# Kernel tuning notes

Measured on AMD Instinct MI355X. Metric: run time of the kernel, lower is better.

## Reference

```python
import jax, jax.numpy as jnp
import numpy as np

B, C, H, W, N = 16, 81, 128, 128, 64


def setup_inputs() -> dict:
    key = jax.random.key(0)
    k1, k2, k3, k4, k5 = jax.random.split(key, 5)
    bbox_pred = jax.random.normal(k1, (B, 4, H, W), jnp.float32)
    class_pred = jax.random.normal(k2, (B, C, H, W), jnp.float32)
    # well-formed GT boxes in [0,1]: x1y1 + positive wh
    xy = jax.random.uniform(k3, (B, N, 2), jnp.float32)
    wh = jax.random.uniform(k4, (B, N, 2), jnp.float32) * 0.5 + 0.05
    boxes = jnp.concatenate([xy, xy + wh], axis=-1)  # [B,N,4]
    labels = jax.random.randint(k5, (B, N), 0, C).astype(jnp.int32)
    return {"bbox_pred": bbox_pred, "class_pred": class_pred,
            "boxes": boxes, "labels": labels}


def reference(bbox_pred, class_pred, boxes, labels):
    Bb, Cc, Hh, Ww = class_pred.shape
    A = Hh * Ww
    pb = bbox_pred.transpose(0, 2, 3, 1).reshape(Bb, A, 4)   # [B,A,4]
    pc = class_pred.transpose(0, 2, 3, 1).reshape(Bb, A, Cc)  # [B,A,C]

    # pairwise IoU [B,A,N] via broadcasting (pred [B,A,1,4] vs gt [B,1,N,4])
    p = pb[:, :, None, :]
    g = boxes[:, None, :, :]
    ix1 = jnp.maximum(p[..., 0], g[..., 0])
    iy1 = jnp.maximum(p[..., 1], g[..., 1])
    ix2 = jnp.minimum(p[..., 2], g[..., 2])
    iy2 = jnp.minimum(p[..., 3], g[..., 3])
    inter = jnp.clip(ix2 - ix1, 0) * jnp.clip(iy2 - iy1, 0)
    pa = (pb[..., 2] - pb[..., 0]) * (pb[..., 3] - pb[..., 1])      # [B,A]
    ga = (boxes[..., 2] - boxes[..., 0]) * (boxes[..., 3] - boxes[..., 1])  # [B,N]
    union = pa[:, :, None] + ga[:, None, :] - inter
    ious = inter / union

    max_ious = ious.max(axis=-1)            # [B,A]
    max_idx = jnp.argmax(ious, axis=-1)     # [B,A]
    pos = max_ious > 0.5                    # [B,A]
    posf = pos.astype(pc.dtype)
    npos = posf.sum(axis=-1)                # [B]
    denom = jnp.maximum(npos, 1.0)

    assigned_labels = jnp.take_along_axis(labels, max_idx, axis=1)          # [B,A]
    assigned_boxes = jnp.take_along_axis(boxes, max_idx[..., None], axis=1)  # [B,A,4]

    # cross-entropy per anchor (mean over positives)
    logp = jax.nn.log_softmax(pc, axis=-1)
    ce = -jnp.take_along_axis(logp, assigned_labels[..., None], axis=2)[..., 0]
    cls_loss = (ce * posf).sum(axis=-1) / denom

    # smooth-L1 (beta=1), mean over positive elements (npos*4)
    diff = pb - assigned_boxes
    ad = jnp.abs(diff)
    sl1 = jnp.where(ad < 1.0, 0.5 * diff * diff, ad - 0.5)
    reg_loss = (sl1 * posf[..., None]).sum(axis=(-1, -2)) / (denom * 4.0)

    # fallback when an image has zero positives: CE with all-zero labels
    zero_loss = -logp[..., 0].mean(axis=-1)

    per_img = jnp.where(npos > 0, cls_loss + reg_loss, zero_loss)
    return per_img.mean()
```

## Files before the change

kernel.cpp:

```cpp
#include <hip/hip_runtime.h>
#include <math.h>

#define Bc 16
#define Cc 81
#define AA 16384
#define Nn 64
#define TPB 256
#define BLOCKS_PER_IMG (AA / TPB)
#define NBLOCKS (Bc * BLOCKS_PER_IMG)
#define G 9
#define NG 9

__global__ __launch_bounds__(TPB) void det_loss_main(
    const float* __restrict__ bbox_pred,
    const float* __restrict__ class_pred,
    const float* __restrict__ boxes,
    const int* __restrict__ labels,
    float4* __restrict__ ws_part)
{
    __shared__ float4 sbox[Nn];
    __shared__ float  sga[Nn];
    __shared__ int    slab[Nn];

    const int blk  = blockIdx.x;
    const int b    = blk / BLOCKS_PER_IMG;
    const int ablk = blk % BLOCKS_PER_IMG;
    const int t    = threadIdx.x;

    if (t < Nn) {
        float4 g = ((const float4*)boxes)[b * Nn + t];
        sbox[t] = g;
        sga[t]  = (g.z - g.x) * (g.w - g.y);
        slab[t] = labels[b * Nn + t];
    }
    __syncthreads();

    const int a = ablk * TPB + t;

    const float* bp = bbox_pred + (size_t)b * 4 * AA + a;
    const float px1 = bp[0 * AA];
    const float py1 = bp[1 * AA];
    const float px2 = bp[2 * AA];
    const float py2 = bp[3 * AA];
    const float pa  = (px2 - px1) * (py2 - py1);

    const float* cp = class_pred + (size_t)b * Cc * AA + a;
    float buf0[G], buf1[G];
#pragma unroll
    for (int k = 0; k < G; ++k) buf0[k] = cp[(size_t)k * AA];

    float best = -INFINITY;
    int   bj   = 0;
#pragma unroll 8
    for (int j = 0; j < Nn; ++j) {
        const float4 g  = sbox[j];
        const float ix1 = fmaxf(px1, g.x);
        const float iy1 = fmaxf(py1, g.y);
        const float ix2 = fminf(px2, g.z);
        const float iy2 = fminf(py2, g.w);
        const float inter = fmaxf(ix2 - ix1, 0.0f) * fmaxf(iy2 - iy1, 0.0f);
        const float iou = inter * __builtin_amdgcn_rcpf(pa + sga[j] - inter);
        if (iou > best) { best = iou; bj = j; }
    }
    const float posf = (best > 0.5f) ? 1.0f : 0.0f;
    const int    lab = slab[bj];
    const float4 gb  = sbox[bj];

    float sA = 0.0f, sB = 0.0f, x0 = 0.0f, xl = 0.0f;
#pragma unroll
    for (int g = 0; g < NG; ++g) {
        if (g + 1 < NG) {
            if ((g & 1) == 0) {
#pragma unroll
                for (int k = 0; k < G; ++k)
                    buf1[k] = cp[(size_t)((g + 1) * G + k) * AA];
            } else {
#pragma unroll
                for (int k = 0; k < G; ++k)
                    buf0[k] = cp[(size_t)((g + 1) * G + k) * AA];
            }
        }
#pragma unroll
        for (int k = 0; k < G; ++k) {
            const float x = ((g & 1) == 0) ? buf0[k] : buf1[k];
            const int   c = g * G + k;
            if (c == 0) x0 = x;
            xl = (c == lab) ? x : xl;
            if (k & 1) sB += __expf(x);
            else       sA += __expf(x);
        }
    }
    const float lse   = __logf(sA + sB);
    const float ce    = (lse - xl) * posf;
    const float logp0 = x0 - lse;

    float sl = 0.0f;
    {
        const float d0 = px1 - gb.x, d1 = py1 - gb.y, d2 = px2 - gb.z, d3 = py2 - gb.w;
        const float a0 = fabsf(d0), a1 = fabsf(d1), a2 = fabsf(d2), a3 = fabsf(d3);
        sl += (a0 < 1.0f) ? 0.5f * d0 * d0 : a0 - 0.5f;
        sl += (a1 < 1.0f) ? 0.5f * d1 * d1 : a1 - 0.5f;
        sl += (a2 < 1.0f) ? 0.5f * d2 * d2 : a2 - 0.5f;
        sl += (a3 < 1.0f) ? 0.5f * d3 * d3 : a3 - 0.5f;
        sl *= posf;
    }

    float v0 = posf, v1 = ce, v2 = sl, v3 = logp0;
#pragma unroll
    for (int o = 32; o > 0; o >>= 1) {
        v0 += __shfl_down(v0, o);
        v1 += __shfl_down(v1, o);
        v2 += __shfl_down(v2, o);
        v3 += __shfl_down(v3, o);
    }
    __shared__ float4 red[4];
    const int wave = t >> 6, lane = t & 63;
    if (lane == 0) red[wave] = make_float4(v0, v1, v2, v3);
    __syncthreads();
    if (t == 0) {
        float4 r0 = red[0], r1 = red[1], r2 = red[2], r3 = red[3];
        ws_part[blk] = make_float4(r0.x + r1.x + r2.x + r3.x,
                                   r0.y + r1.y + r2.y + r3.y,
                                   r0.z + r1.z + r2.z + r3.z,
                                   r0.w + r1.w + r2.w + r3.w);
    }
}

__global__ __launch_bounds__(256) void det_loss_final(
    const float4* __restrict__ ws_part, float* __restrict__ out)
{
    const int t = threadIdx.x;
    float4 p0 = ws_part[t];
    float4 p1 = ws_part[t + 256];
    float4 p2 = ws_part[t + 512];
    float4 p3 = ws_part[t + 768];
#pragma unroll
    for (int o = 1; o < 64; o <<= 1) {
        p0.x += __shfl_xor(p0.x, o); p0.y += __shfl_xor(p0.y, o);
        p0.z += __shfl_xor(p0.z, o); p0.w += __shfl_xor(p0.w, o);
        p1.x += __shfl_xor(p1.x, o); p1.y += __shfl_xor(p1.y, o);
        p1.z += __shfl_xor(p1.z, o); p1.w += __shfl_xor(p1.w, o);
        p2.x += __shfl_xor(p2.x, o); p2.y += __shfl_xor(p2.y, o);
        p2.z += __shfl_xor(p2.z, o); p2.w += __shfl_xor(p2.w, o);
        p3.x += __shfl_xor(p3.x, o); p3.y += __shfl_xor(p3.y, o);
        p3.z += __shfl_xor(p3.z, o); p3.w += __shfl_xor(p3.w, o);
    }
    __shared__ float4 simg[16];
    const int lane = t & 63, w = t >> 6;
    if (lane == 0) {
        simg[w]      = p0;
        simg[w + 4]  = p1;
        simg[w + 8]  = p2;
        simg[w + 12] = p3;
    }
    __syncthreads();
    float per = 0.0f;
    if (t < Bc) {
        const float4 s = simg[t];
        const float npos = s.x;
        const float denom = fmaxf(npos, 1.0f);
        const float cls_reg = s.y / denom + s.z / (denom * 4.0f);
        const float zero_loss = -s.w / (float)AA;
        per = (npos > 0.0f) ? cls_reg : zero_loss;
    }
#pragma unroll
    for (int o = 8; o > 0; o >>= 1) per += __shfl_down(per, o);
    if (t == 0) out[0] = per * (1.0f / (float)Bc);
}

extern "C" void kernel_launch(void* const* d_in, const int* in_sizes, int n_in,
                              void* d_out, int out_size, void* d_ws, size_t ws_size,
                              hipStream_t stream) {
    const float* bbox_pred  = (const float*)d_in[0];
    const float* class_pred = (const float*)d_in[1];
    const float* boxes      = (const float*)d_in[2];
    const int*   labels     = (const int*)d_in[3];
    float* out = (float*)d_out;
    float4* ws = (float4*)d_ws;

    det_loss_main<<<NBLOCKS, TPB, 0, stream>>>(bbox_pred, class_pred, boxes, labels, ws);
    det_loss_final<<<1, 256, 0, stream>>>(ws, out);
}
```

Before: 24.49 us.

## Stream class logits through LDS with async global_load_lds double buffering

Replaces per-thread register-buffered strided loads of the 81 class rows with async global-to-LDS copies (16-byte per lane) into a double-buffered 16-row chunk in shared memory, synchronized via manual waitcnt and barriers. The first two chunks are issued before the IoU loop so the logit loads overlap the IoU computation, and the last row is loaded directly. This frees registers and widens the load granularity, but adds 32KB of LDS per block and block-wide barriers, which may reduce occupancy.

```diff
diff --git a/kernel.cpp b/kernel.cpp
--- a/kernel.cpp
+++ b/kernel.cpp
@@ -8,8 +8,22 @@
 #define TPB 256
 #define BLOCKS_PER_IMG (AA / TPB)
 #define NBLOCKS (Bc * BLOCKS_PER_IMG)
-#define G 9
-#define NG 9
+#define CHROWS 16
+#define NCHUNK 5
+
+__device__ __forceinline__ void issue_chunk(const float* __restrict__ cp_anchor,
+                                            float (*chk)[CHROWS][TPB],
+                                            int ci, int bi, int w, int l) {
+#pragma unroll
+    for (int r = 0; r < 4; ++r) {
+        const int c = ci * CHROWS + 4 * w + r;
+        const float* gp = cp_anchor + (size_t)c * AA + 4 * l;
+        __builtin_amdgcn_global_load_lds(
+            (const __attribute__((address_space(1))) unsigned int*)gp,
+            (__attribute__((address_space(3))) unsigned int*)&chk[bi][4 * w + r][0],
+            16, 0, 0);
+    }
+}
 
 __global__ __launch_bounds__(TPB) void det_loss_main(
     const float* __restrict__ bbox_pred,
@@ -21,11 +35,16 @@
     __shared__ float4 sbox[Nn];
     __shared__ float  sga[Nn];
     __shared__ int    slab[Nn];
+    __shared__ __align__(16) float chk[2][CHROWS][TPB];
+    __shared__ float4 red[4];
 
     const int blk  = blockIdx.x;
     const int b    = blk / BLOCKS_PER_IMG;
     const int ablk = blk % BLOCKS_PER_IMG;
     const int t    = threadIdx.x;
+    const int w    = t >> 6;
+    const int l    = t & 63;
+    const int base = ablk * TPB;
 
     if (t < Nn) {
         float4 g = ((const float4*)boxes)[b * Nn + t];
@@ -35,19 +54,18 @@
     }
     __syncthreads();
 
-    const int a = ablk * TPB + t;
-
-    const float* bp = bbox_pred + (size_t)b * 4 * AA + a;
+    const float* bp = bbox_pred + (size_t)b * 4 * AA + base + t;
     const float px1 = bp[0 * AA];
     const float py1 = bp[1 * AA];
     const float px2 = bp[2 * AA];
     const float py2 = bp[3 * AA];
     const float pa  = (px2 - px1) * (py2 - py1);
 
-    const float* cp = class_pred + (size_t)b * Cc * AA + a;
-    float buf0[G], buf1[G];
-#pragma unroll
-    for (int k = 0; k < G; ++k) buf0[k] = cp[(size_t)k * AA];
+    const float* cp_anchor = class_pred + (size_t)b * Cc * AA + base;
+    issue_chunk(cp_anchor, chk, 0, 0, w, l);
+    issue_chunk(cp_anchor, chk, 1, 1, w, l);
+    __builtin_amdgcn_sched_barrier(0);
+    const float x80 = cp_anchor[(size_t)80 * AA + t];
 
     float best = -INFINITY;
     int   bj   = 0;
@@ -66,30 +84,43 @@
     const int    lab = slab[bj];
     const float4 gb  = sbox[bj];
 
+    asm volatile("s_waitcnt vmcnt(4)" ::: "memory");
+    __builtin_amdgcn_sched_barrier(0);
+    __builtin_amdgcn_s_barrier();
+    __builtin_amdgcn_sched_barrier(0);
+
     float sA = 0.0f, sB = 0.0f, x0 = 0.0f, xl = 0.0f;
 #pragma unroll
-    for (int g = 0; g < NG; ++g) {
-        if (g + 1 < NG) {
-            if ((g & 1) == 0) {
-#pragma unroll
-                for (int k = 0; k < G; ++k)
-                    buf1[k] = cp[(size_t)((g + 1) * G + k) * AA];
-            } else {
-#pragma unroll
-                for (int k = 0; k < G; ++k)
-                    buf0[k] = cp[(size_t)((g + 1) * G + k) * AA];
-            }
-        }
-#pragma unroll
-        for (int k = 0; k < G; ++k) {
-            const float x = ((g & 1) == 0) ? buf0[k] : buf1[k];
-            const int   c = g * G + k;
+    for (int i = 0; i < 4; ++i) {
+#pragma unroll
+        for (int r = 0; r < CHROWS; ++r) {
+            const float x = chk[i & 1][r][t];
+            const int   c = i * CHROWS + r;
             if (c == 0) x0 = x;
             xl = (c == lab) ? x : xl;
-            if (k & 1) sB += __expf(x);
+            if (r & 1) sB += __expf(x);
             else       sA += __expf(x);
         }
-    }
+        __builtin_amdgcn_s_barrier();
+        __builtin_amdgcn_sched_barrier(0);
+        if (i < 3) issue_chunk(cp_anchor, chk, i + 2, i & 1, w, l);
+        if (i < 3) asm volatile("s_waitcnt vmcnt(4)" ::: "memory");
+        else       asm volatile("s_waitcnt vmcnt(0)" ::: "memory");
+        __builtin_amdgcn_sched_barrier(0);
+        __builtin_amdgcn_s_barrier();
+        __builtin_amdgcn_sched_barrier(0);
+    }
+#pragma unroll
+    for (int r = 0; r < CHROWS; ++r) {
+        const float x = chk[0][r][t];
+        const int   c = 4 * CHROWS + r;
+        xl = (c == lab) ? x : xl;
+        if (r & 1) sB += __expf(x);
+        else       sA += __expf(x);
+    }
+    xl = (lab == 80) ? x80 : xl;
+    sA += __expf(x80);
+
     const float lse   = __logf(sA + sB);
     const float ce    = (lse - xl) * posf;
     const float logp0 = x0 - lse;
@@ -113,9 +144,7 @@
         v2 += __shfl_down(v2, o);
         v3 += __shfl_down(v3, o);
     }
-    __shared__ float4 red[4];
-    const int wave = t >> 6, lane = t & 63;
-    if (lane == 0) red[wave] = make_float4(v0, v1, v2, v3);
+    if (l == 0) red[w] = make_float4(v0, v1, v2, v3);
     __syncthreads();
     if (t == 0) {
         float4 r0 = red[0], r1 = red[1], r2 = red[2], r3 = red[3];
```

Result: slower. 26.89 us (+9.8%).

## Split class dimension across two thread halves per anchor to double parallelism

Applied to the files above, without the earlier changes.

Each block now covers 128 anchors with 256 threads. Two waves split the 81 classes (40 and 41 each) for the same anchors and combine partial sum-exp and label logit through shared memory. This doubles the thread count and the number of in-flight loads while halving the serial exp/load chain per thread. The cost is that the IoU argmax is computed twice per anchor, an extra barrier is needed, and the final reduction now reads twice as many partials.

```diff
diff --git a/kernel.cpp b/kernel.cpp
--- a/kernel.cpp
+++ b/kernel.cpp
@@ -6,12 +6,13 @@
 #define AA 16384
 #define Nn 64
 #define TPB 256
-#define BLOCKS_PER_IMG (AA / TPB)
+#define APB 128
+#define BLOCKS_PER_IMG (AA / APB)
 #define NBLOCKS (Bc * BLOCKS_PER_IMG)
-#define G 9
-#define NG 9
+#define G 8
+#define NG 5
 
-__global__ __launch_bounds__(TPB) void det_loss_main(
+__global__ __launch_bounds__(TPB, 8) void det_loss_main(
     const float* __restrict__ bbox_pred,
     const float* __restrict__ class_pred,
     const float* __restrict__ boxes,
@@ -21,11 +22,19 @@
     __shared__ float4 sbox[Nn];
     __shared__ float  sga[Nn];
     __shared__ int    slab[Nn];
+    __shared__ float  s_sum1[APB];
+    __shared__ float  s_xl1[APB];
+    __shared__ float4 red[4];
 
     const int blk  = blockIdx.x;
     const int b    = blk / BLOCKS_PER_IMG;
     const int ablk = blk % BLOCKS_PER_IMG;
     const int t    = threadIdx.x;
+    const int w    = t >> 6;
+    const int l    = t & 63;
+    const int half = w >> 1;
+    const int ai   = ((w & 1) << 6) | l;
+    const int a    = ablk * APB + ai;
 
     if (t < Nn) {
         float4 g = ((const float4*)boxes)[b * Nn + t];
@@ -35,8 +44,6 @@
     }
     __syncthreads();
 
-    const int a = ablk * TPB + t;
-
     const float* bp = bbox_pred + (size_t)b * 4 * AA + a;
     const float px1 = bp[0 * AA];
     const float py1 = bp[1 * AA];
@@ -44,10 +51,13 @@
     const float py2 = bp[3 * AA];
     const float pa  = (px2 - px1) * (py2 - py1);
 
-    const float* cp = class_pred + (size_t)b * Cc * AA + a;
+    const float* cp = class_pred + ((size_t)b * Cc + half * 40) * AA + a;
     float buf0[G], buf1[G];
 #pragma unroll
     for (int k = 0; k < G; ++k) buf0[k] = cp[(size_t)k * AA];
+#pragma unroll
+    for (int k = 0; k < G; ++k) buf1[k] = cp[(size_t)(G + k) * AA];
+    const float x80v = cp[(size_t)40 * AA];
 
     float best = -INFINITY;
     int   bj   = 0;
@@ -66,46 +76,54 @@
     const int    lab = slab[bj];
     const float4 gb  = sbox[bj];
 
-    float sA = 0.0f, sB = 0.0f, x0 = 0.0f, xl = 0.0f;
+    float s = 0.0f, xl = 0.0f, x0 = 0.0f;
 #pragma unroll
     for (int g = 0; g < NG; ++g) {
-        if (g + 1 < NG) {
-            if ((g & 1) == 0) {
+        const bool even = (g & 1) == 0;
 #pragma unroll
-                for (int k = 0; k < G; ++k)
-                    buf1[k] = cp[(size_t)((g + 1) * G + k) * AA];
+        for (int k = 0; k < G; ++k) {
+            const float x = even ? buf0[k] : buf1[k];
+            const int   c = half * 40 + g * G + k;
+            if (half == 0 && g == 0 && k == 0) x0 = x;
+            xl = (c == lab) ? x : xl;
+            s += __expf(x);
+        }
+        if (g + 2 < NG) {
+            if (even) {
+#pragma unroll
+                for (int k = 0; k < G; ++k) buf0[k] = cp[(size_t)((g + 2) * G + k) * AA];
             } else {
 #pragma unroll
-                for (int k = 0; k < G; ++k)
-                    buf0[k] = cp[(size_t)((g + 1) * G + k) * AA];
+                for (int k = 0; k < G; ++k) buf1[k] = cp[(size_t)((g + 2) * G + k) * AA];
             }
         }
-#pragma unroll
-        for (int k = 0; k < G; ++k) {
-            const float x = ((g & 1) == 0) ? buf0[k] : buf1[k];
-            const int   c = g * G + k;
-            if (c == 0) x0 = x;
-            xl = (c == lab) ? x : xl;
-            if (k & 1) sB += __expf(x);
-            else       sA += __expf(x);
-        }
     }
-    const float lse   = __logf(sA + sB);
-    const float ce    = (lse - xl) * posf;
-    const float logp0 = x0 - lse;
+    if (half == 1) {
+        xl = (lab == 80) ? x80v : xl;
+        s += __expf(x80v);
+    }
 
-    float sl = 0.0f;
-    {
+    if (half == 1) { s_sum1[ai] = s; s_xl1[ai] = xl; }
+    __syncthreads();
+
+    float v0 = 0.0f, v1 = 0.0f, v2 = 0.0f, v3 = 0.0f;
+    if (half == 0) {
+        const float sumexp = s + s_sum1[ai];
+        const float xlt    = xl + s_xl1[ai];
+        const float lse    = __logf(sumexp);
+        v0 = posf;
+        v1 = (lse - xlt) * posf;
+        v3 = x0 - lse;
+        float sl = 0.0f;
         const float d0 = px1 - gb.x, d1 = py1 - gb.y, d2 = px2 - gb.z, d3 = py2 - gb.w;
         const float a0 = fabsf(d0), a1 = fabsf(d1), a2 = fabsf(d2), a3 = fabsf(d3);
         sl += (a0 < 1.0f) ? 0.5f * d0 * d0 : a0 - 0.5f;
         sl += (a1 < 1.0f) ? 0.5f * d1 * d1 : a1 - 0.5f;
         sl += (a2 < 1.0f) ? 0.5f * d2 * d2 : a2 - 0.5f;
         sl += (a3 < 1.0f) ? 0.5f * d3 * d3 : a3 - 0.5f;
-        sl *= posf;
+        v2 = sl * posf;
     }
 
-    float v0 = posf, v1 = ce, v2 = sl, v3 = logp0;
 #pragma unroll
     for (int o = 32; o > 0; o >>= 1) {
         v0 += __shfl_down(v0, o);
@@ -113,9 +131,7 @@
         v2 += __shfl_down(v2, o);
         v3 += __shfl_down(v3, o);
     }
-    __shared__ float4 red[4];
-    const int wave = t >> 6, lane = t & 63;
-    if (lane == 0) red[wave] = make_float4(v0, v1, v2, v3);
+    if (l == 0) red[w] = make_float4(v0, v1, v2, v3);
     __syncthreads();
     if (t == 0) {
         float4 r0 = red[0], r1 = red[1], r2 = red[2], r3 = red[3];
@@ -130,37 +146,31 @@
     const float4* __restrict__ ws_part, float* __restrict__ out)
 {
     const int t = threadIdx.x;
-    float4 p0 = ws_part[t];
-    float4 p1 = ws_part[t + 256];
-    float4 p2 = ws_part[t + 512];
-    float4 p3 = ws_part[t + 768];
+    const int w = t >> 6, lane = t & 63;
+    float4 p[8];
+#pragma unroll
+    for (int r = 0; r < 8; ++r) p[r] = ws_part[t + 256 * r];
 #pragma unroll
     for (int o = 1; o < 64; o <<= 1) {
-        p0.x += __shfl_xor(p0.x, o); p0.y += __shfl_xor(p0.y, o);
-        p0.z += __shfl_xor(p0.z, o); p0.w += __shfl_xor(p0.w, o);
-        p1.x += __shfl_xor(p1.x, o); p1.y += __shfl_xor(p1.y, o);
-        p1.z += __shfl_xor(p1.z, o); p1.w += __shfl_xor(p1.w, o);
-        p2.x += __shfl_xor(p2.x, o); p2.y += __shfl_xor(p2.y, o);
-        p2.z += __shfl_xor(p2.z, o); p2.w += __shfl_xor(p2.w, o);
-        p3.x += __shfl_xor(p3.x, o); p3.y += __shfl_xor(p3.y, o);
-        p3.z += __shfl_xor(p3.z, o); p3.w += __shfl_xor(p3.w, o);
+#pragma unroll
+        for (int r = 0; r < 8; ++r) {
+            p[r].x += __shfl_xor(p[r].x, o); p[r].y += __shfl_xor(p[r].y, o);
+            p[r].z += __shfl_xor(p[r].z, o); p[r].w += __shfl_xor(p[r].w, o);
+        }
     }
-    __shared__ float4 simg[16];
-    const int lane = t & 63, w = t >> 6;
+    __shared__ float4 part[16][2];
     if (lane == 0) {
-        simg[w]      = p0;
-        simg[w + 4]  = p1;
-        simg[w + 8]  = p2;
-        simg[w + 12] = p3;
+#pragma unroll
+        for (int r = 0; r < 8; ++r) part[2 * r + (w >> 1)][w & 1] = p[r];
     }
     __syncthreads();
     float per = 0.0f;
     if (t < Bc) {
-        const float4 s = simg[t];
-        const float npos = s.x;
+        const float4 sa = part[t][0], sb = part[t][1];
+        const float npos = sa.x + sb.x;
         const float denom = fmaxf(npos, 1.0f);
-        const float cls_reg = s.y / denom + s.z / (denom * 4.0f);
-        const float zero_loss = -s.w / (float)AA;
+        const float cls_reg = (sa.y + sb.y) / denom + (sa.z + sb.z) / (denom * 4.0f);
+        const float zero_loss = -(sa.w + sb.w) / (float)AA;
         per = (npos > 0.0f) ? cls_reg : zero_loss;
     }
 #pragma unroll
```

Result: slower. 33.52 us (+36.9%).
